# Performance work log

Measured on AMD Instinct MI355X. Metric: run time of the kernel, lower is better.

The kernel has to match this reference:

```python
import jax, jax.numpy as jnp
import numpy as np
from jax import lax

N_C = 2
T = 5
NE = 17   # equality constraints per (sample, t)
NV = 24   # variables per (sample, t): p(4), f(4), f_e(4), alpha1(2), alpha2(2), gamma(4), gamma_e(4)
ITERS = 400
B = 512

F_MASK = jnp.zeros((NV,), bool).at[4:8].set(True)     # L1-penalized coords (f)
NN_MASK = jnp.zeros((NV,), bool).at[12:24].set(True)  # nonneg coords (alpha1, alpha2, gamma, gamma_e)


def _conv(x, w, b):
    return lax.conv_general_dilated(x, w, (1, 1), 'VALID',
                                    dimension_numbers=('NCHW', 'OIHW', 'NCHW')) + b[None, :, None, None]


def _maxpool(x, k):
    return lax.reduce_window(x, -jnp.inf, lax.max, (1, 1, k, k), (1, 1, k, k), 'VALID')


def _encoder(img, cw1, cb1, cw2, cb2, w3, b3, w4, b4):
    h = jax.nn.relu(_maxpool(_conv(img, cw1, cb1), 2))   # (B,10,20,20)
    h = jax.nn.relu(_maxpool(_conv(h, cw2, cb2), 4))     # (B,20,4,4)
    h = h.reshape(h.shape[0], -1)                        # (B,320)
    h = jax.nn.relu(h @ w3.T + b3)                       # dropout is eval-mode identity
    return jax.nn.relu(h @ w4.T + b4)                    # (B,100)


def _mlp(h, w1, b1, w2, b2, w3, b3):
    h = jax.nn.relu(h @ w1.T + b1)  # dropout eval-mode identity
    h = jax.nn.relu(h @ w2.T + b2)
    return h @ w3.T + b3


def _build_Ab(r, ddr, fc, p_e, fc_e, v, p_r):
    # one (t)-slice: r(3), ddr(3), fc(8), p_e(4), fc_e(8), v(8), p_r(4) -> A(17,24), b(17)
    A = jnp.zeros((NE, NV))
    b = jnp.zeros((NE,))
    # force balance x: sum(f) + f_e0 + f_e1 = ddr0  (original f[:20] covers all 4 rows, f[20:] empty)
    A = A.at[0, 4:8].set(1.0).at[0, 8].set(1.0).at[0, 9].set(1.0)
    b = b.at[0].set(ddr[0])
    # force balance y: f_e2 + f_e3 = ddr1
    A = A.at[1, 10].set(1.0).at[1, 11].set(1.0)
    b = b.at[1].set(ddr[1])
    # torque balance
    A = A.at[2, 6].set(p_r[0] - r[0]).at[2, 4].set(-(p_r[2] - r[1]))
    A = A.at[2, 7].set(p_r[1] - r[0]).at[2, 5].set(-(p_r[3] - r[1]))
    A = A.at[2, 10].set(p_e[0] - r[0]).at[2, 8].set(-(p_e[2] - r[1]))
    A = A.at[2, 11].set(p_e[1] - r[0]).at[2, 9].set(-(p_e[3] - r[1]))
    b = b.at[2].set(ddr[2])
    for c in range(N_C):
        # p = alpha1*v_a + alpha2*v_b, alpha1+alpha2=1
        A = A.at[3 + 3 * c, c].set(1.0).at[3 + 3 * c, 12 + c].set(-v[2 * c]).at[3 + 3 * c, 14 + c].set(-v[2 * c + 2])
        A = A.at[4 + 3 * c, c + 2].set(1.0).at[4 + 3 * c, 12 + c].set(-v[2 * c + 1]).at[4 + 3 * c, 14 + c].set(-v[2 * c + 3])
        A = A.at[5 + 3 * c, 12 + c].set(1.0).at[5 + 3 * c, 14 + c].set(1.0)
        b = b.at[5 + 3 * c].set(1.0)
        # friction cone: f = gamma1*fc_a + gamma2*fc_b
        A = A.at[9 + 2 * c, 16 + c].set(fc[2 * c]).at[9 + 2 * c, 18 + c].set(fc[2 * c + 2]).at[9 + 2 * c, 4 + c].set(-1.0)
        A = A.at[10 + 2 * c, 16 + c].set(fc[2 * c + 1]).at[10 + 2 * c, 18 + c].set(fc[2 * c + 3]).at[10 + 2 * c, 6 + c].set(-1.0)
    # external force cones
    A = A.at[13, 20].set(fc_e[0]).at[13, 21].set(fc_e[2]).at[13, 8].set(-1.0)
    A = A.at[14, 20].set(fc_e[1]).at[14, 21].set(fc_e[3]).at[14, 10].set(-1.0)
    A = A.at[15, 22].set(fc_e[4]).at[15, 23].set(fc_e[6]).at[15, 9].set(-1.0)
    A = A.at[16, 22].set(fc_e[5]).at[16, 23].set(fc_e[7]).at[16, 11].set(-1.0)
    return A, b


def _specnorm(A):
    def body(i, u):
        u = A.T @ (A @ u)
        return u / (jnp.linalg.norm(u) + 1e-12)
    u = lax.fori_loop(0, 25, body, jnp.ones((A.shape[-1],), A.dtype))
    return jnp.linalg.norm(A @ u)


def _solve_lp(A, b):
    # batched: min ||f||_1  s.t.  A z = b,  z[nn] >= 0   via PDHG (Chambolle-Pock)
    P = A.shape[0]
    L = lax.stop_gradient(jax.vmap(_specnorm)(A))
    tau = (0.9 / (L + 1e-8))[:, None]
    sig = tau

    def step(carry, _):
        z, zb, y = carry
        y = y + sig * (jnp.einsum('pev,pv->pe', A, zb) - b)
        g = z - tau * jnp.einsum('pev,pe->pv', A, y)
        zn = jnp.where(F_MASK, jnp.sign(g) * jnp.maximum(jnp.abs(g) - tau, 0.0),
                       jnp.where(NN_MASK, jnp.maximum(g, 0.0), g))
        return (zn, 2.0 * zn - z, y), None

    z0 = jnp.zeros((P, NV))
    y0 = jnp.zeros((P, NE))
    (z, _, _), _ = lax.scan(step, (z0, z0, y0), None, length=ITERS)
    return z


def reference(xtraj, x, x_img, cw1, cb1, cw2, cb2, w3, b3, w4, b4,
              pw1, pb1, pw2, pb2, pw3, pb3, vw1, vb1, vw2, vb2, vw3, vb3):
    Bn = xtraj.shape[0]
    img = x_img.reshape(Bn, 1, 50, 50)
    e = _encoder(img, cw1, cb1, cw2, cb2, w3, b3, w4, b4)       # (B,100)
    h = jnp.concatenate([e, xtraj], axis=1)                     # (B,145)
    p_r = _mlp(h, pw1, pb1, pw2, pb2, pw3, pb3)                 # (B,20)
    v = _mlp(h, vw1, vb1, vw2, vb2, vw3, vb3)                   # (B,40)
    r = xtraj[:, :15].reshape(Bn, 3, T)
    ddr = xtraj[:, 30:45].reshape(Bn, 3, T)
    fc = x[:, 20:60].reshape(Bn, 8, T)
    p_e = x[:, 60:80].reshape(Bn, 4, T)
    fc_e = x[:, 80:120].reshape(Bn, 8, T)
    vM = v.reshape(Bn, 8, T)
    p_rM = p_r.reshape(Bn, 4, T)

    def flat(a):  # (B,d,T) -> (B*T, d)
        return jnp.swapaxes(a, 1, 2).reshape(Bn * T, a.shape[1])

    A, bvec = jax.vmap(_build_Ab)(flat(r), flat(ddr), flat(fc), flat(p_e), flat(fc_e), flat(vM), flat(p_rM))
    z = _solve_lp(A, bvec).reshape(Bn, T, NV)
    p = jnp.swapaxes(z[..., 0:4], 1, 2).reshape(Bn, 20)   # matches p.view(1,-1) C-order of (4,5)
    f = jnp.swapaxes(z[..., 4:8], 1, 2).reshape(Bn, 20)
    dp = p_r - x[:, 0:20]
    dv = v - x[:, 120:160]
    return 100.0 * jnp.concatenate([p, f, 10.0 * dp, 10.0 * dv], axis=1)  # (B,100)


def setup_inputs() -> dict:
    key = jax.random.key(0)
    ks = jax.random.split(key, 32)

    def rn(k, shape, s=0.05):
        return (s * jax.random.normal(k, shape)).astype(jnp.float32)

    return {
        'xtraj': rn(ks[0], (B, 45), 1.0),
        'x': rn(ks[1], (B, 160), 1.0),
        'x_img': rn(ks[2], (B, 2500), 1.0),
        'cw1': rn(ks[3], (10, 1, 11, 11)), 'cb1': rn(ks[4], (10,)),
        'cw2': rn(ks[5], (20, 10, 5, 5)), 'cb2': rn(ks[6], (20,)),
        'w3': rn(ks[7], (150, 320)), 'b3': rn(ks[8], (150,)),
        'w4': rn(ks[9], (100, 150)), 'b4': rn(ks[10], (100,)),
        'pw1': rn(ks[11], (100, 145)), 'pb1': rn(ks[12], (100,)),
        'pw2': rn(ks[13], (100, 100)), 'pb2': rn(ks[14], (100,)),
        'pw3': rn(ks[15], (20, 100)), 'pb3': rn(ks[16], (20,)),
        'vw1': rn(ks[17], (100, 145)), 'vb1': rn(ks[18], (100,)),
        'vw2': rn(ks[19], (100, 100)), 'vb2': rn(ks[20], (100,)),
        'vw3': rn(ks[21], (40, 100)), 'vb3': rn(ks[22], (40,)),
    }
```

## Files before the change

kernel.cpp:

```cpp
#include <hip/hip_runtime.h>

__global__ __launch_bounds__(128) void conv1_kernel(
    const float* __restrict__ x_img, const float* __restrict__ cw1,
    const float* __restrict__ cb1, float* __restrict__ h1)
{
    const int blk = blockIdx.x;
    const int b = blk >> 2;
    const int c = blk & 3;
    const int tid = threadIdx.x;

    __shared__ __align__(16) float s_img[1000];

    const float* img = x_img + (size_t)b * 2500 + (size_t)(10 * c) * 50;
    for (int i = tid; i < 1000; i += 128) s_img[i] = img[i];
    __syncthreads();

    if (tid < 100) {
        const int ly = tid / 20, px = tid % 20;
        const int py = 5 * c + ly;
        const int C = 2 * px;
        float acc0[10], acc1[10], acc2[10], acc3[10];
        #pragma unroll
        for (int oc = 0; oc < 10; ++oc) { acc0[oc] = 0.f; acc1[oc] = 0.f; acc2[oc] = 0.f; acc3[oc] = 0.f; }
        for (int r = 0; r < 12; ++r) {
            float v[12];
            #pragma unroll
            for (int j = 0; j < 6; ++j) {
                float2 t = *(const float2*)&s_img[(2 * ly + r) * 50 + C + 2 * j];
                v[2 * j] = t.x; v[2 * j + 1] = t.y;
            }
            if (r < 11) {
                #pragma unroll
                for (int oc = 0; oc < 10; ++oc) {
                    #pragma unroll
                    for (int kx = 0; kx < 11; ++kx) {
                        float w0 = cw1[oc * 121 + r * 11 + kx];
                        acc0[oc] = fmaf(v[kx], w0, acc0[oc]);
                        acc1[oc] = fmaf(v[kx + 1], w0, acc1[oc]);
                    }
                }
            }
            if (r >= 1) {
                #pragma unroll
                for (int oc = 0; oc < 10; ++oc) {
                    #pragma unroll
                    for (int kx = 0; kx < 11; ++kx) {
                        float w1 = cw1[oc * 121 + (r - 1) * 11 + kx];
                        acc2[oc] = fmaf(v[kx], w1, acc2[oc]);
                        acc3[oc] = fmaf(v[kx + 1], w1, acc3[oc]);
                    }
                }
            }
        }
        float* hb = h1 + (size_t)b * 4000 + py * 20 + px;
        #pragma unroll
        for (int oc = 0; oc < 10; ++oc) {
            float m = fmaxf(fmaxf(acc0[oc], acc1[oc]), fmaxf(acc2[oc], acc3[oc]));
            hb[oc * 400] = fmaxf(m + cb1[oc], 0.f);
        }
    }
}

__global__ __launch_bounds__(320) void head_kernel(
    const float* __restrict__ xtraj, const float* __restrict__ x,
    const float* __restrict__ h1g,
    const float* __restrict__ cw2, const float* __restrict__ cb2,
    const float* __restrict__ w3, const float* __restrict__ b3,
    const float* __restrict__ w4, const float* __restrict__ b4,
    const float* __restrict__ pw1, const float* __restrict__ pb1,
    const float* __restrict__ pw2, const float* __restrict__ pb2,
    const float* __restrict__ pw3, const float* __restrict__ pb3,
    const float* __restrict__ vw1, const float* __restrict__ vb1,
    const float* __restrict__ vw2, const float* __restrict__ vb2,
    const float* __restrict__ vw3, const float* __restrict__ vb3,
    float* __restrict__ out, float* __restrict__ ws_pr, float* __restrict__ ws_v)
{
    const int b = blockIdx.x;
    const int tid = threadIdx.x;

    __shared__ __align__(16) float s_h1[4000];
    __shared__ __align__(16) float s_w2[5000];
    __shared__ __align__(16) float s_h2[320];
    __shared__ float s_hc[145];
    __shared__ float s_t1[152];
    __shared__ float s_m1[256];
    __shared__ float s_m2[256];

    {
        const float4* src = (const float4*)(h1g + (size_t)b * 4000);
        float4* dst = (float4*)s_h1;
        for (int i = tid; i < 1000; i += 320) dst[i] = src[i];
        const float4* wsrc = (const float4*)cw2;
        float4* wdst = (float4*)s_w2;
        for (int i = tid; i < 1250; i += 320) wdst[i] = wsrc[i];
    }
    __syncthreads();

    {
        const int oc = tid >> 4, cell = tid & 15;
        const int R0 = (cell >> 2) * 4, C0 = (cell & 3) * 4;
        float acc[16];
        #pragma unroll
        for (int i = 0; i < 16; ++i) acc[i] = 0.f;
        for (int ic = 0; ic < 10; ++ic) {
            const float* hb = &s_h1[ic * 400];
            const float* wb = &s_w2[oc * 250 + ic * 25];
            float v[8][8];
            #pragma unroll
            for (int r = 0; r < 8; ++r) {
                float4 t0 = *(const float4*)&hb[(R0 + r) * 20 + C0];
                float4 t1 = *(const float4*)&hb[(R0 + r) * 20 + C0 + 4];
                v[r][0] = t0.x; v[r][1] = t0.y; v[r][2] = t0.z; v[r][3] = t0.w;
                v[r][4] = t1.x; v[r][5] = t1.y; v[r][6] = t1.z; v[r][7] = t1.w;
            }
            #pragma unroll
            for (int k = 0; k < 5; ++k) {
                #pragma unroll
                for (int kx = 0; kx < 5; ++kx) {
                    float wv = wb[k * 5 + kx];
                    #pragma unroll
                    for (int o = 0; o < 4; ++o) {
                        #pragma unroll
                        for (int cc = 0; cc < 4; ++cc)
                            acc[o * 4 + cc] = fmaf(v[o + k][cc + kx], wv, acc[o * 4 + cc]);
                    }
                }
            }
        }
        float m = acc[0];
        #pragma unroll
        for (int i = 1; i < 16; ++i) m = fmaxf(m, acc[i]);
        s_h2[tid] = fmaxf(m + cb2[oc], 0.f);
    }
    __syncthreads();

    if (tid < 150) {
        const float* w = w3 + tid * 320;
        float a0 = b3[tid], a1 = 0.f, a2 = 0.f, a3 = 0.f;
        for (int k = 0; k < 320; k += 4) {
            a0 = fmaf(s_h2[k],     w[k],     a0);
            a1 = fmaf(s_h2[k + 1], w[k + 1], a1);
            a2 = fmaf(s_h2[k + 2], w[k + 2], a2);
            a3 = fmaf(s_h2[k + 3], w[k + 3], a3);
        }
        s_t1[tid] = fmaxf((a0 + a1) + (a2 + a3), 0.f);
    }
    __syncthreads();

    if (tid < 100) {
        const float* w = w4 + tid * 150;
        float a0 = b4[tid], a1 = 0.f;
        for (int k = 0; k < 150; k += 2) {
            a0 = fmaf(s_t1[k],     w[k],     a0);
            a1 = fmaf(s_t1[k + 1], w[k + 1], a1);
        }
        s_hc[tid] = fmaxf(a0 + a1, 0.f);
    }
    if (tid >= 100 && tid < 145) s_hc[tid] = xtraj[b * 45 + (tid - 100)];
    __syncthreads();

    if (tid < 100) {
        const float* w = pw1 + tid * 145;
        float acc = pb1[tid];
        for (int k = 0; k < 145; ++k) acc = fmaf(s_hc[k], w[k], acc);
        s_m1[tid] = fmaxf(acc, 0.f);
    } else if (tid >= 128 && tid < 228) {
        int i = tid - 128;
        const float* w = vw1 + i * 145;
        float acc = vb1[i];
        for (int k = 0; k < 145; ++k) acc = fmaf(s_hc[k], w[k], acc);
        s_m1[tid] = fmaxf(acc, 0.f);
    }
    __syncthreads();

    if (tid < 100) {
        const float* w = pw2 + tid * 100;
        float acc = pb2[tid];
        for (int k = 0; k < 100; ++k) acc = fmaf(s_m1[k], w[k], acc);
        s_m2[tid] = fmaxf(acc, 0.f);
    } else if (tid >= 128 && tid < 228) {
        int i = tid - 128;
        const float* w = vw2 + i * 100;
        float acc = vb2[i];
        for (int k = 0; k < 100; ++k) acc = fmaf(s_m1[128 + k], w[k], acc);
        s_m2[tid] = fmaxf(acc, 0.f);
    }
    __syncthreads();

    if (tid < 20) {
        const float* w = pw3 + tid * 100;
        float acc = pb3[tid];
        for (int k = 0; k < 100; ++k) acc = fmaf(s_m2[k], w[k], acc);
        ws_pr[b * 20 + tid] = acc;
        out[b * 100 + 40 + tid] = 1000.f * (acc - x[b * 160 + tid]);
    } else if (tid >= 128 && tid < 168) {
        int i = tid - 128;
        const float* w = vw3 + i * 100;
        float acc = vb3[i];
        for (int k = 0; k < 100; ++k) acc = fmaf(s_m2[128 + k], w[k], acc);
        ws_v[b * 40 + i] = acc;
        out[b * 100 + 60 + i] = 1000.f * (acc - x[b * 160 + 120 + i]);
    }
}

__device__ const signed char AZ_IDX[32][8] = {
    {4,5,6,7,8,9,0,0},{10,11,0,0,0,0,0,0},{4,5,6,7,8,9,10,11},
    {0,12,14,0,0,0,0,0},{2,12,14,0,0,0,0,0},{12,14,0,0,0,0,0,0},
    {1,13,15,0,0,0,0,0},{3,13,15,0,0,0,0,0},{13,15,0,0,0,0,0,0},
    {16,18,4,0,0,0,0,0},{16,18,6,0,0,0,0,0},{17,19,5,0,0,0,0,0},
    {17,19,7,0,0,0,0,0},{20,21,8,0,0,0,0,0},{20,21,10,0,0,0,0,0},
    {22,23,9,0,0,0,0,0},{22,23,11,0,0,0,0,0},
    {0},{0},{0},{0},{0},{0},{0},{0},{0},{0},{0},{0},{0},{0},{0}
};
__device__ const signed char AZ_SEL[32][8] = {
    {1,1,1,1,1,1,0,0},{1,1,0,0,0,0,0,0},{3,4,5,6,7,8,9,10},
    {1,11,13,0,0,0,0,0},{1,12,14,0,0,0,0,0},{1,1,0,0,0,0,0,0},
    {1,13,15,0,0,0,0,0},{1,14,16,0,0,0,0,0},{1,1,0,0,0,0,0,0},
    {17,19,2,0,0,0,0,0},{18,20,2,0,0,0,0,0},{19,21,2,0,0,0,0,0},
    {20,22,2,0,0,0,0,0},{23,25,2,0,0,0,0,0},{24,26,2,0,0,0,0,0},
    {27,29,2,0,0,0,0,0},{28,30,2,0,0,0,0,0},
    {0},{0},{0},{0},{0},{0},{0},{0},{0},{0},{0},{0},{0},{0},{0}
};
__device__ const signed char AT_IDX[32][3] = {
    {3,0,0},{6,0,0},{4,0,0},{7,0,0},
    {0,2,9},{0,2,11},{0,2,10},{0,2,12},{0,2,13},{0,2,15},{1,2,14},{1,2,16},
    {3,4,5},{6,7,8},{3,4,5},{6,7,8},
    {9,10,0},{11,12,0},{9,10,0},{11,12,0},
    {13,14,0},{13,14,0},{15,16,0},{15,16,0},
    {0},{0},{0},{0},{0},{0},{0},{0}
};
__device__ const signed char AT_SEL[32][3] = {
    {1,0,0},{1,0,0},{1,0,0},{1,0,0},
    {1,3,2},{1,4,2},{1,5,2},{1,6,2},{1,7,2},{1,8,2},{1,9,2},{1,10,2},
    {11,12,1},{13,14,1},{13,14,1},{15,16,1},
    {17,18,0},{19,20,0},{19,20,0},{21,22,0},
    {23,24,0},{25,26,0},{27,28,0},{29,30,0},
    {0},{0},{0},{0},{0},{0},{0},{0}
};

__global__ __launch_bounds__(64) void lp_kernel(
    const float* __restrict__ xtraj, const float* __restrict__ x,
    const float* __restrict__ ws_pr, const float* __restrict__ ws_v,
    float* __restrict__ out, int nprob)
{
    const int g = threadIdx.x >> 5;
    const int l = threadIdx.x & 31;
    const int p = blockIdx.x * 2 + g;
    const int pc = p < nprob ? p : nprob - 1;
    const int b = pc / 5, t = pc % 5;
    const float* xt = xtraj + b * 45;
    const float* xb = x + b * 160;

    __shared__ float s_val[2][32];

    {
        float val = 0.f;
        if (l == 1) val = 1.f;
        else if (l == 2) val = -1.f;
        else if (l >= 3 && l <= 10) {
            float r0 = xt[t], r1 = xt[5 + t];
            switch (l) {
                case 3:  val = r1 - ws_pr[b * 20 + 10 + t]; break;
                case 4:  val = r1 - ws_pr[b * 20 + 15 + t]; break;
                case 5:  val = ws_pr[b * 20 + 0 + t] - r0;  break;
                case 6:  val = ws_pr[b * 20 + 5 + t] - r0;  break;
                case 7:  val = r1 - xb[60 + 10 + t]; break;
                case 8:  val = r1 - xb[60 + 15 + t]; break;
                case 9:  val = xb[60 + 0 + t] - r0;  break;
                default: val = xb[60 + 5 + t] - r0;  break;
            }
        }
        else if (l >= 11 && l <= 16) val = -ws_v[b * 40 + 5 * (l - 11) + t];
        else if (l >= 17 && l <= 22) val = xb[20 + 5 * (l - 17) + t];
        else if (l >= 23 && l <= 30) val = xb[80 + 5 * (l - 23) + t];
        s_val[g][l] = val;
    }
    __syncthreads();

    float cfA[8]; int ixA[8];
    #pragma unroll
    for (int k = 0; k < 8; ++k) {
        ixA[k] = AZ_IDX[l][k];
        cfA[k] = s_val[g][(int)AZ_SEL[l][k]];
    }
    float cfT[3]; int ixT[3];
    #pragma unroll
    for (int k = 0; k < 3; ++k) {
        ixT[k] = AT_IDX[l][k];
        cfT[k] = s_val[g][(int)AT_SEL[l][k]];
    }
    float bb = 0.f;
    if (l == 0) bb = xt[30 + t];
    else if (l == 1) bb = xt[35 + t];
    else if (l == 2) bb = xt[40 + t];
    else if (l == 5 || l == 8) bb = 1.f;

    const bool isF  = (l >= 4 && l < 8);
    const bool isNN = (l >= 12);

    float u = (l < 24) ? 1.f : 0.f;
    for (int it = 0; it < 25; ++it) {
        float w = 0.f;
        #pragma unroll
        for (int k = 0; k < 8; ++k) w = fmaf(cfA[k], __shfl(u, ixA[k], 32), w);
        float nu = 0.f;
        #pragma unroll
        for (int k = 0; k < 3; ++k) nu = fmaf(cfT[k], __shfl(w, ixT[k], 32), nu);
        float s = (l < 24) ? nu * nu : 0.f;
        s += __shfl_xor(s, 16, 32); s += __shfl_xor(s, 8, 32);
        s += __shfl_xor(s, 4, 32);  s += __shfl_xor(s, 2, 32);
        s += __shfl_xor(s, 1, 32);
        u = nu / (sqrtf(s) + 1e-12f);
    }
    float tau;
    {
        float w = 0.f;
        #pragma unroll
        for (int k = 0; k < 8; ++k) w = fmaf(cfA[k], __shfl(u, ixA[k], 32), w);
        float s2 = (l < 17) ? w * w : 0.f;
        s2 += __shfl_xor(s2, 16, 32); s2 += __shfl_xor(s2, 8, 32);
        s2 += __shfl_xor(s2, 4, 32);  s2 += __shfl_xor(s2, 2, 32);
        s2 += __shfl_xor(s2, 1, 32);
        tau = 0.9f / (sqrtf(s2) + 1e-8f);
    }

    float zv = 0.f, zbv = 0.f, yv = 0.f;
    for (int it = 0; it < 400; ++it) {
        float w = 0.f;
        #pragma unroll
        for (int k = 0; k < 8; ++k) w = fmaf(cfA[k], __shfl(zbv, ixA[k], 32), w);
        yv = fmaf(tau, w - bb, yv);

        float gv = 0.f;
        #pragma unroll
        for (int k = 0; k < 3; ++k) gv = fmaf(cfT[k], __shfl(yv, ixT[k], 32), gv);

        float gg = fmaf(-tau, gv, zv);
        float st = copysignf(fmaxf(fabsf(gg) - tau, 0.f), gg);
        float nn = fmaxf(gg, 0.f);
        float zn = isF ? st : (isNN ? nn : gg);
        zbv = 2.f * zn - zv;
        zv = zn;
    }

    if (p < nprob) {
        float* ob = out + b * 100;
        if (l < 4)      ob[l * 5 + t]            = 100.f * zv;
        else if (l < 8) ob[20 + (l - 4) * 5 + t] = 100.f * zv;
    }
}

extern "C" void kernel_launch(void* const* d_in, const int* in_sizes, int n_in,
                              void* d_out, int out_size, void* d_ws, size_t ws_size,
                              hipStream_t stream) {
    const float* xtraj = (const float*)d_in[0];
    const float* x     = (const float*)d_in[1];
    const float* x_img = (const float*)d_in[2];
    const float* cw1 = (const float*)d_in[3];
    const float* cb1 = (const float*)d_in[4];
    const float* cw2 = (const float*)d_in[5];
    const float* cb2 = (const float*)d_in[6];
    const float* w3  = (const float*)d_in[7];
    const float* b3  = (const float*)d_in[8];
    const float* w4  = (const float*)d_in[9];
    const float* b4  = (const float*)d_in[10];
    const float* pw1 = (const float*)d_in[11];
    const float* pb1 = (const float*)d_in[12];
    const float* pw2 = (const float*)d_in[13];
    const float* pb2 = (const float*)d_in[14];
    const float* pw3 = (const float*)d_in[15];
    const float* pb3 = (const float*)d_in[16];
    const float* vw1 = (const float*)d_in[17];
    const float* vb1 = (const float*)d_in[18];
    const float* vw2 = (const float*)d_in[19];
    const float* vb2 = (const float*)d_in[20];
    const float* vw3 = (const float*)d_in[21];
    const float* vb3 = (const float*)d_in[22];

    float* out = (float*)d_out;
    const int Bn = in_sizes[0] / 45;

    float* ws_pr = (float*)d_ws;
    float* ws_v  = ws_pr + (size_t)Bn * 20;
    float* ws_h1 = ws_v + (size_t)Bn * 40;

    conv1_kernel<<<Bn * 4, 128, 0, stream>>>(x_img, cw1, cb1, ws_h1);

    head_kernel<<<Bn, 320, 0, stream>>>(
        xtraj, x, ws_h1, cw2, cb2, w3, b3, w4, b4,
        pw1, pb1, pw2, pb2, pw3, pb3, vw1, vb1, vw2, vb2, vw3, vb3,
        out, ws_pr, ws_v);

    const int nprob = Bn * 5;
    lp_kernel<<<(nprob + 1) / 2, 64, 0, stream>>>(xtraj, x, ws_pr, ws_v, out, nprob);
}
```

Before: 275.4 us.

## Precompute A^T A in the LP solver to merge the two sparse matvecs

The LP solver kernel now builds A and b in shared memory and precomputes the sparse Gram matrix A^T A, up to 10 entries per row, along with A^T b. Each primal-dual iteration then runs one sparse matvec on z-bar with a dual accumulator q = A^T y. This replaces the two dependent shuffle-matvecs (A, then A^T). The power iteration and the step-size estimate use the Gram matrix as well. This shortens the serial shuffle chain per iteration (8+3 dependent shuffles become 10 independent ones) at the cost of some setup work and shared memory, and it slightly changes floating-point rounding.

```diff
diff --git a/kernel.cpp b/kernel.cpp
--- a/kernel.cpp
+++ b/kernel.cpp
@@ -229,12 +229,58 @@
     {13,14,0},{13,14,0},{15,16,0},{15,16,0},
     {0},{0},{0},{0},{0},{0},{0},{0}
 };
-__device__ const signed char AT_SEL[32][3] = {
-    {1,0,0},{1,0,0},{1,0,0},{1,0,0},
-    {1,3,2},{1,4,2},{1,5,2},{1,6,2},{1,7,2},{1,8,2},{1,9,2},{1,10,2},
-    {11,12,1},{13,14,1},{13,14,1},{15,16,1},
-    {17,18,0},{19,20,0},{19,20,0},{21,22,0},
-    {23,24,0},{25,26,0},{27,28,0},{29,30,0},
+__device__ const signed char M_IDX[32][10] = {
+    {0,12,14,0,0,0,0,0,0,0},
+    {1,13,15,0,0,0,0,0,0,0},
+    {2,12,14,0,0,0,0,0,0,0},
+    {3,13,15,0,0,0,0,0,0,0},
+    {4,5,6,7,8,9,10,11,16,18},
+    {4,5,6,7,8,9,10,11,17,19},
+    {4,5,6,7,8,9,10,11,16,18},
+    {4,5,6,7,8,9,10,11,17,19},
+    {4,5,6,7,8,9,10,11,20,21},
+    {4,5,6,7,8,9,10,11,22,23},
+    {4,5,6,7,8,9,10,11,20,21},
+    {4,5,6,7,8,9,10,11,22,23},
+    {0,2,12,14,0,0,0,0,0,0},
+    {1,3,13,15,0,0,0,0,0,0},
+    {0,2,12,14,0,0,0,0,0,0},
+    {1,3,13,15,0,0,0,0,0,0},
+    {4,6,16,18,0,0,0,0,0,0},
+    {5,7,17,19,0,0,0,0,0,0},
+    {4,6,16,18,0,0,0,0,0,0},
+    {5,7,17,19,0,0,0,0,0,0},
+    {8,10,20,21,0,0,0,0,0,0},
+    {8,10,20,21,0,0,0,0,0,0},
+    {9,11,22,23,0,0,0,0,0,0},
+    {9,11,22,23,0,0,0,0,0,0},
+    {0},{0},{0},{0},{0},{0},{0},{0}
+};
+__device__ const signed char M_MSK[32][10] = {
+    {1,1,1,0,0,0,0,0,0,0},
+    {1,1,1,0,0,0,0,0,0,0},
+    {1,1,1,0,0,0,0,0,0,0},
+    {1,1,1,0,0,0,0,0,0,0},
+    {1,1,1,1,1,1,1,1,1,1},
+    {1,1,1,1,1,1,1,1,1,1},
+    {1,1,1,1,1,1,1,1,1,1},
+    {1,1,1,1,1,1,1,1,1,1},
+    {1,1,1,1,1,1,1,1,1,1},
+    {1,1,1,1,1,1,1,1,1,1},
+    {1,1,1,1,1,1,1,1,1,1},
+    {1,1,1,1,1,1,1,1,1,1},
+    {1,1,1,1,0,0,0,0,0,0},
+    {1,1,1,1,0,0,0,0,0,0},
+    {1,1,1,1,0,0,0,0,0,0},
+    {1,1,1,1,0,0,0,0,0,0},
+    {1,1,1,1,0,0,0,0,0,0},
+    {1,1,1,1,0,0,0,0,0,0},
+    {1,1,1,1,0,0,0,0,0,0},
+    {1,1,1,1,0,0,0,0,0,0},
+    {1,1,1,1,0,0,0,0,0,0},
+    {1,1,1,1,0,0,0,0,0,0},
+    {1,1,1,1,0,0,0,0,0,0},
+    {1,1,1,1,0,0,0,0,0,0},
     {0},{0},{0},{0},{0},{0},{0},{0}
 };
 
@@ -252,6 +298,8 @@
     const float* xb = x + b * 160;
 
     __shared__ float s_val[2][32];
+    __shared__ float s_A[2][17][24];
+    __shared__ float s_b[2][17];
 
     {
         float val = 0.f;
@@ -275,25 +323,41 @@
         else if (l >= 23 && l <= 30) val = xb[80 + 5 * (l - 23) + t];
         s_val[g][l] = val;
     }
-    __syncthreads();
-
-    float cfA[8]; int ixA[8];
+    for (int i = threadIdx.x; i < 2 * 17 * 24; i += 64) (&s_A[0][0][0])[i] = 0.f;
+    __syncthreads();
+
+    if (l < 17) {
+        #pragma unroll
+        for (int k = 0; k < 8; ++k) {
+            int sel = AZ_SEL[l][k];
+            if (sel != 0) s_A[g][l][(int)AZ_IDX[l][k]] = s_val[g][sel];
+        }
+        float bb = 0.f;
+        if (l == 0) bb = xt[30 + t];
+        else if (l == 1) bb = xt[35 + t];
+        else if (l == 2) bb = xt[40 + t];
+        else if (l == 5 || l == 8) bb = 1.f;
+        s_b[g][l] = bb;
+    }
+    __syncthreads();
+
+    float mcf[10];
+    int midx[10];
+    float cc = 0.f;
     #pragma unroll
-    for (int k = 0; k < 8; ++k) {
-        ixA[k] = AZ_IDX[l][k];
-        cfA[k] = s_val[g][(int)AZ_SEL[l][k]];
-    }
-    float cfT[3]; int ixT[3];
-    #pragma unroll
-    for (int k = 0; k < 3; ++k) {
-        ixT[k] = AT_IDX[l][k];
-        cfT[k] = s_val[g][(int)AT_SEL[l][k]];
-    }
-    float bb = 0.f;
-    if (l == 0) bb = xt[30 + t];
-    else if (l == 1) bb = xt[35 + t];
-    else if (l == 2) bb = xt[40 + t];
-    else if (l == 5 || l == 8) bb = 1.f;
+    for (int k = 0; k < 10; ++k) { mcf[k] = 0.f; midx[k] = 0; }
+    if (l < 24) {
+        int e0 = AT_IDX[l][0], e1 = AT_IDX[l][1], e2 = AT_IDX[l][2];
+        float a0 = s_A[g][e0][l], a1 = s_A[g][e1][l], a2 = s_A[g][e2][l];
+        cc = a0 * s_b[g][e0] + a1 * s_b[g][e1] + a2 * s_b[g][e2];
+        #pragma unroll
+        for (int k = 0; k < 10; ++k) {
+            int j = M_IDX[l][k];
+            midx[k] = j;
+            float m = a0 * s_A[g][e0][j] + a1 * s_A[g][e1][j] + a2 * s_A[g][e2][j];
+            mcf[k] = (M_MSK[l][k] != 0) ? m : 0.f;
+        }
+    }
 
     const bool isF  = (l >= 4 && l < 8);
     const bool isNN = (l >= 12);
@@ -302,40 +366,33 @@
     for (int it = 0; it < 25; ++it) {
         float w = 0.f;
         #pragma unroll
-        for (int k = 0; k < 8; ++k) w = fmaf(cfA[k], __shfl(u, ixA[k], 32), w);
-        float nu = 0.f;
-        #pragma unroll
-        for (int k = 0; k < 3; ++k) nu = fmaf(cfT[k], __shfl(w, ixT[k], 32), nu);
-        float s = (l < 24) ? nu * nu : 0.f;
+        for (int k = 0; k < 10; ++k) w = fmaf(mcf[k], __shfl(u, midx[k], 32), w);
+        float s = w * w;
         s += __shfl_xor(s, 16, 32); s += __shfl_xor(s, 8, 32);
         s += __shfl_xor(s, 4, 32);  s += __shfl_xor(s, 2, 32);
         s += __shfl_xor(s, 1, 32);
-        u = nu / (sqrtf(s) + 1e-12f);
+        u = w / (sqrtf(s) + 1e-12f);
     }
     float tau;
     {
         float w = 0.f;
         #pragma unroll
-        for (int k = 0; k < 8; ++k) w = fmaf(cfA[k], __shfl(u, ixA[k], 32), w);
-        float s2 = (l < 17) ? w * w : 0.f;
+        for (int k = 0; k < 10; ++k) w = fmaf(mcf[k], __shfl(u, midx[k], 32), w);
+        float s2 = u * w;
         s2 += __shfl_xor(s2, 16, 32); s2 += __shfl_xor(s2, 8, 32);
         s2 += __shfl_xor(s2, 4, 32);  s2 += __shfl_xor(s2, 2, 32);
         s2 += __shfl_xor(s2, 1, 32);
-        tau = 0.9f / (sqrtf(s2) + 1e-8f);
-    }
-
-    float zv = 0.f, zbv = 0.f, yv = 0.f;
+        tau = 0.9f / (sqrtf(fmaxf(s2, 0.f)) + 1e-8f);
+    }
+
+    float zv = 0.f, zbv = 0.f, qv = 0.f;
     for (int it = 0; it < 400; ++it) {
-        float w = 0.f;
-        #pragma unroll
-        for (int k = 0; k < 8; ++k) w = fmaf(cfA[k], __shfl(zbv, ixA[k], 32), w);
-        yv = fmaf(tau, w - bb, yv);
-
-        float gv = 0.f;
-        #pragma unroll
-        for (int k = 0; k < 3; ++k) gv = fmaf(cfT[k], __shfl(yv, ixT[k], 32), gv);
-
-        float gg = fmaf(-tau, gv, zv);
+        float s = 0.f;
+        #pragma unroll
+        for (int k = 0; k < 10; ++k) s = fmaf(mcf[k], __shfl(zbv, midx[k], 32), s);
+        qv = fmaf(tau, s - cc, qv);
+
+        float gg = fmaf(-tau, qv, zv);
         float st = copysignf(fmaxf(fabsf(gg) - tau, 0.f), gg);
         float nn = fmaxf(gg, 0.f);
         float zn = isF ? st : (isNN ? nn : gg);
```

Measured after the change: 268.0 us. -2.7%, faster.
